# Performance work log

Hardware: AMD Instinct MI355X
Metric: run time of the kernel (lower is better)

The kernel has to match this reference:

```python
import jax, jax.numpy as jnp
import numpy as np

L, H, D, FF = 6, 12, 768, 3072  # num_layers, nhead, d_model, dim_feedforward
B, N = 4, 1024                  # batch, tokens
EPS = 1e-5                      # LayerNorm eps (torch default)


def setup_inputs() -> dict:
    key = jax.random.key(0)
    ks = jax.random.split(key, 6)
    s = 0.02
    return {
        "x": jax.random.normal(ks[0], (B, N, D), jnp.float32),
        "Wqkv": jax.random.normal(ks[1], (L, 3 * D, D), jnp.float32) * s,
        "bqkv": jnp.zeros((L, 3 * D), jnp.float32),
        "Wo": jax.random.normal(ks[2], (L, D, D), jnp.float32) * s,
        "bo": jnp.zeros((L, D), jnp.float32),
        "ln1_g": jnp.ones((L, D), jnp.float32),
        "ln1_b": jnp.zeros((L, D), jnp.float32),
        "ln2_g": jnp.ones((L, D), jnp.float32),
        "ln2_b": jnp.zeros((L, D), jnp.float32),
        "W1": jax.random.normal(ks[3], (L, FF, D), jnp.float32) * s,
        "b1": jnp.zeros((L, FF), jnp.float32),
        "W2": jax.random.normal(ks[4], (L, D, FF), jnp.float32) * s,
        "b2": jnp.zeros((L, D), jnp.float32),
    }


def _ln(x, g, b):
    m = jnp.mean(x, axis=-1, keepdims=True)
    v = jnp.var(x, axis=-1, keepdims=True)
    return (x - m) * jax.lax.rsqrt(v + EPS) * g + b


def _mha(x, Wqkv, bqkv, Wo, bo):
    # nn.MultiheadAttention with need_weights=True: explicit QK^T-softmax-AV path
    b_, n_, d_ = x.shape
    dh = d_ // H
    qkv = x @ Wqkv.T + bqkv                       # [B, N, 3D]
    q, k, v = jnp.split(qkv, 3, axis=-1)
    heads = lambda t: t.reshape(b_, n_, H, dh).transpose(0, 2, 1, 3)  # [B, H, N, dh]
    q, k, v = heads(q), heads(k), heads(v)
    scores = jnp.einsum('bhnd,bhmd->bhnm', q, k) / jnp.sqrt(jnp.float32(dh))
    attn = jax.nn.softmax(scores, axis=-1)        # [B, H, N, N] (the captured weights)
    out = jnp.einsum('bhnm,bhmd->bhnd', attn, v)
    out = out.transpose(0, 2, 1, 3).reshape(b_, n_, d_)
    return out @ Wo.T + bo


def reference(x, Wqkv, bqkv, Wo, bo, ln1_g, ln1_b, ln2_g, ln2_b, W1, b1, W2, b2):
    # Faithful to the custom forward: norm1 -> MHA -> residual -> norm1 again -> FFN -> residual -> norm2
    # dropout=0.0 (eval), so dropout layers are identity.
    for l in range(L):
        src = _ln(x, ln1_g[l], ln1_b[l])
        a = _mha(src, Wqkv[l], bqkv[l], Wo[l], bo[l])
        x = _ln(x + a, ln1_g[l], ln1_b[l])
        h = jax.nn.gelu(x @ W1[l].T + b1[l], approximate=False)  # torch 'gelu' = exact erf gelu
        x = _ln(x + h @ W2[l].T + b2[l], ln2_g[l], ln2_b[l])
    return x
```

## Files before the change

### kernel.cpp

```cpp
#include <hip/hip_runtime.h>
#include <math.h>

#define DEV __device__ __forceinline__

typedef __attribute__((ext_vector_type(4))) float f32x4;
typedef __attribute__((ext_vector_type(8))) __bf16 bf16x8;
typedef __attribute__((ext_vector_type(4))) unsigned short u16x4;
typedef __attribute__((ext_vector_type(8))) unsigned short u16x8;

enum {
  LAYERS = 6, NH = 12, DM = 768, FFD = 3072, BB = 4, NT = 1024,
  MM = BB * NT,
  TD = 3 * DM
};

DEV unsigned short f2bf(float f) {
  union { float f; unsigned u; } c; c.f = f;
  unsigned u = c.u;
  return (unsigned short)((u + 0x7fffu + ((u >> 16) & 1u)) >> 16);
}

DEV void gll16(const void* gsrc, void* ldst) {
  __builtin_amdgcn_global_load_lds(
      (const __attribute__((address_space(1))) unsigned int*)gsrc,
      (__attribute__((address_space(3))) unsigned int*)ldst, 16, 0, 0);
}

DEV f32x4 mfma16(bf16x8 a, bf16x8 b, f32x4 c) {
  return __builtin_amdgcn_mfma_f32_16x16x32_bf16(a, b, c, 0, 0, 0);
}

__global__ __launch_bounds__(256) void cvt_kernel(const f32x4* __restrict__ in,
                                                  u16x4* __restrict__ out, int n4) {
  int i = blockIdx.x * blockDim.x + threadIdx.x;
  int stride = gridDim.x * blockDim.x;
  for (; i < n4; i += stride) {
    f32x4 v = in[i];
    u16x4 o;
    o[0] = f2bf(v[0]); o[1] = f2bf(v[1]); o[2] = f2bf(v[2]); o[3] = f2bf(v[3]);
    out[i] = o;
  }
}

__global__ __launch_bounds__(256) void ln_kernel(const float* __restrict__ xin,
                                                 const float* __restrict__ ain,
                                                 const float* __restrict__ gam,
                                                 const float* __restrict__ bet,
                                                 float* __restrict__ xout,
                                                 unsigned short* __restrict__ bfout) {
  const int row  = blockIdx.x * 4 + (threadIdx.x >> 6);
  const int lane = threadIdx.x & 63;
  const f32x4* xr = (const f32x4*)(xin + (size_t)row * DM);
  f32x4 v[3];
#pragma unroll
  for (int p = 0; p < 3; p++) v[p] = xr[lane + 64 * p];
  if (ain) {
    const f32x4* ar = (const f32x4*)(ain + (size_t)row * DM);
#pragma unroll
    for (int p = 0; p < 3; p++) v[p] += ar[lane + 64 * p];
  }
  float s = 0.f, sq = 0.f;
#pragma unroll
  for (int p = 0; p < 3; p++)
#pragma unroll
    for (int j = 0; j < 4; j++) { float f = v[p][j]; s += f; sq += f * f; }
#pragma unroll
  for (int o = 1; o < 64; o <<= 1) {
    s  += __shfl_xor(s, o, 64);
    sq += __shfl_xor(sq, o, 64);
  }
  const float mean = s * (1.0f / DM);
  const float var  = sq * (1.0f / DM) - mean * mean;
  const float rstd = rsqrtf(var + 1e-5f);
  const f32x4* gr = (const f32x4*)gam;
  const f32x4* br = (const f32x4*)bet;
#pragma unroll
  for (int p = 0; p < 3; p++) {
    f32x4 gv = gr[lane + 64 * p];
    f32x4 bv = br[lane + 64 * p];
    f32x4 o = (v[p] - mean) * rstd * gv + bv;
    if (xout) ((f32x4*)(xout + (size_t)row * DM))[lane + 64 * p] = o;
    if (bfout) {
      u16x4 h;
      h[0] = f2bf(o[0]); h[1] = f2bf(o[1]); h[2] = f2bf(o[2]); h[3] = f2bf(o[3]);
      ((u16x4*)(bfout + (size_t)row * DM))[lane + 64 * p] = h;
    }
  }
}

template <int EPI, int TN>
__global__ __launch_bounds__(256) void gemm_bt(const unsigned short* __restrict__ A,
                                               const unsigned short* __restrict__ Wb,
                                               const float* __restrict__ bias,
                                               void* __restrict__ Cout,
                                               int Ksz, int Nsz) {
  constexpr int BN = TN / 32;
  __shared__ alignas(16) unsigned short As[128 * 32];
  __shared__ alignas(16) unsigned short Bs[TN * 32];

  const int t = threadIdx.x;
  const int lane = t & 63;
  const int w = t >> 6;
  const int g = lane >> 4;
  const int qi = lane & 15;
  const int wr = w >> 1;
  const int wc = w & 1;
  const int m0 = blockIdx.y * 128;
  const int n0 = blockIdx.x * TN;

  f32x4 acc[4][BN];
#pragma unroll
  for (int am = 0; am < 4; am++)
#pragma unroll
    for (int bn = 0; bn < BN; bn++) acc[am][bn] = (f32x4){0.f, 0.f, 0.f, 0.f};

  const int srow = t >> 2;
  const int schk = t & 3;
  const unsigned short* Ag = A  + (size_t)(m0 + srow) * Ksz + schk * 8;
  const unsigned short* Bg = Wb + (size_t)(n0 + srow) * Ksz + schk * 8;

  for (int kt = 0; kt < Ksz; kt += 32) {
    __syncthreads();
    gll16(Ag + kt,                    As + srow * 32 + schk * 8);
    gll16(Ag + (size_t)64 * Ksz + kt, As + (srow + 64) * 32 + schk * 8);
    gll16(Bg + kt,                    Bs + srow * 32 + schk * 8);
    if constexpr (TN == 128)
      gll16(Bg + (size_t)64 * Ksz + kt, Bs + (srow + 64) * 32 + schk * 8);
    __syncthreads();

    bf16x8 af[4], bfr[BN];
#pragma unroll
    for (int am = 0; am < 4; am++)
      af[am] = *(const bf16x8*)(As + (wr * 64 + am * 16 + qi) * 32 + g * 8);
#pragma unroll
    for (int bn = 0; bn < BN; bn++)
      bfr[bn] = *(const bf16x8*)(Bs + (wc * (TN / 2) + bn * 16 + qi) * 32 + g * 8);
#pragma unroll
    for (int am = 0; am < 4; am++)
#pragma unroll
      for (int bn = 0; bn < BN; bn++)
        acc[am][bn] = mfma16(af[am], bfr[bn], acc[am][bn]);
  }

  float bv[BN];
#pragma unroll
  for (int bn = 0; bn < BN; bn++)
    bv[bn] = bias[n0 + wc * (TN / 2) + bn * 16 + qi];

#pragma unroll
  for (int am = 0; am < 4; am++)
#pragma unroll
    for (int bn = 0; bn < BN; bn++)
#pragma unroll
      for (int r = 0; r < 4; r++) {
        const int mrow = m0 + wr * 64 + am * 16 + g * 4 + r;
        const int ncol = n0 + wc * (TN / 2) + bn * 16 + qi;
        float v = acc[am][bn][r] + bv[bn];
        if constexpr (EPI == 0) {
          ((float*)Cout)[(size_t)mrow * Nsz + ncol] = v;
        } else if constexpr (EPI == 1) {
          if (ncol < DM) v *= 0.125f;
          ((unsigned short*)Cout)[(size_t)mrow * Nsz + ncol] = f2bf(v);
        } else {
          v = 0.5f * v * (1.f + erff(v * 0.70710678118654752f));
          ((unsigned short*)Cout)[(size_t)mrow * Nsz + ncol] = f2bf(v);
        }
      }
}

__global__ __launch_bounds__(128) void attn_kernel(const unsigned short* __restrict__ qkv,
                                                   unsigned short* __restrict__ outp) {
  __shared__ alignas(16) unsigned short Ks[128 * 64];
  __shared__ alignas(16) unsigned short Vt[64 * 128];
  __shared__ alignas(16) unsigned short Ps[2][32 * 128];

  const int t = threadIdx.x;
  const int w = t >> 6;
  const int lane = t & 63;
  const int g = lane >> 4;
  const int qi = lane & 15;
  const int bidx = blockIdx.x;
  const int qtile = bidx & 15;
  const int bh = bidx >> 4;
  const int h = bh % NH;
  const int b = bh / NH;
  const int q0 = qtile * 64 + w * 32;
  const size_t base_bn = (size_t)b * NT;

  bf16x8 qf[2][2];
#pragma unroll
  for (int qt = 0; qt < 2; qt++)
#pragma unroll
    for (int kk = 0; kk < 2; kk++) {
      const int qrow = q0 + qt * 16 + qi;
      qf[qt][kk] = *(const bf16x8*)(qkv + (base_bn + qrow) * TD + h * 64 + kk * 32 + g * 8);
    }

  f32x4 oacc[2][4];
#pragma unroll
  for (int qt = 0; qt < 2; qt++)
#pragma unroll
    for (int dt = 0; dt < 4; dt++) oacc[qt][dt] = (f32x4){0.f, 0.f, 0.f, 0.f};
  float mval[2] = {-__builtin_inff(), -__builtin_inff()};
  float lval[2] = {0.f, 0.f};
  unsigned short* Pw = &Ps[w][0];

  for (int kv0 = 0; kv0 < NT; kv0 += 128) {
    __syncthreads();
#pragma unroll
    for (int rr = 0; rr < 8; rr++) {
      const int n = rr * 16 + (t >> 3);
      const int cd = t & 7;
      const int cg = cd ^ (n & 7);
      const unsigned short* src = qkv + (base_bn + kv0 + n) * TD + DM + h * 64 + cg * 8;
      gll16(src, Ks + n * 64 + cd * 8);
    }
#pragma unroll
    for (int r2 = 0; r2 < 2; r2++) {
      const int kb = t >> 3;
      const int d0 = r2 * 32 + (t & 7) * 4;
      u16x4 vv[8];
#pragma unroll
      for (int i = 0; i < 8; i++)
        vv[i] = *(const u16x4*)(qkv + (base_bn + kv0 + kb * 8 + i) * TD + 2 * DM + h * 64 + d0);
#pragma unroll
      for (int j = 0; j < 4; j++) {
        const int d = d0 + j;
        u16x8 w8;
#pragma unroll
        for (int i = 0; i < 8; i++) w8[i] = vv[i][j];
        *(u16x8*)((char*)Vt + d * 256 + ((kb ^ (d & 7)) * 16)) = w8;
      }
    }
    __syncthreads();

    f32x4 sacc[8][2];
#pragma unroll
    for (int nt = 0; nt < 8; nt++)
#pragma unroll
      for (int qt = 0; qt < 2; qt++) sacc[nt][qt] = (f32x4){0.f, 0.f, 0.f, 0.f};
#pragma unroll
    for (int nt = 0; nt < 8; nt++) {
      const int n = nt * 16 + qi;
      bf16x8 kf0 = *(const bf16x8*)((const char*)Ks + n * 128 + (((0 + g) ^ (n & 7)) * 16));
      bf16x8 kf1 = *(const bf16x8*)((const char*)Ks + n * 128 + (((4 + g) ^ (n & 7)) * 16));
#pragma unroll
      for (int qt = 0; qt < 2; qt++) {
        sacc[nt][qt] = mfma16(kf0, qf[qt][0], sacc[nt][qt]);
        sacc[nt][qt] = mfma16(kf1, qf[qt][1], sacc[nt][qt]);
      }
    }

#pragma unroll
    for (int qt = 0; qt < 2; qt++) {
      float mx = -__builtin_inff();
#pragma unroll
      for (int nt = 0; nt < 8; nt++)
#pragma unroll
        for (int r = 0; r < 4; r++) mx = fmaxf(mx, sacc[nt][qt][r]);
      mx = fmaxf(mx, __shfl_xor(mx, 16, 64));
      mx = fmaxf(mx, __shfl_xor(mx, 32, 64));
      const float mnew = fmaxf(mval[qt], mx);
      const float scl = __expf(mval[qt] - mnew);
      mval[qt] = mnew;
      float rsum = 0.f;
#pragma unroll
      for (int nt = 0; nt < 8; nt++)
#pragma unroll
        for (int r = 0; r < 4; r++) {
          const float p = __expf(sacc[nt][qt][r] - mnew);
          sacc[nt][qt][r] = p;
          rsum += p;
        }
      rsum += __shfl_xor(rsum, 16, 64);
      rsum += __shfl_xor(rsum, 32, 64);
      lval[qt] = lval[qt] * scl + rsum;
#pragma unroll
      for (int r = 0; r < 4; r++) {
        const float sr = __shfl(scl, g * 4 + r, 64);
#pragma unroll
        for (int dt = 0; dt < 4; dt++) oacc[qt][dt][r] *= sr;
      }
      const int qrow = qt * 16 + qi;
#pragma unroll
      for (int nt = 0; nt < 8; nt++) {
        u16x4 pk;
#pragma unroll
        for (int r = 0; r < 4; r++) pk[r] = f2bf(sacc[nt][qt][r]);
        const int byteoff = qrow * 256 + (((2 * nt + (g >> 1)) ^ (qrow & 7)) * 16) + (g & 1) * 8;
        *(u16x4*)((char*)Pw + byteoff) = pk;
      }
    }

#pragma unroll
    for (int kk2 = 0; kk2 < 4; kk2++) {
      bf16x8 pf[2], vf[4];
#pragma unroll
      for (int qt = 0; qt < 2; qt++) {
        const int qrow = qt * 16 + qi;
        pf[qt] = *(const bf16x8*)((const char*)Pw + qrow * 256 + (((kk2 * 4 + g) ^ (qrow & 7)) * 16));
      }
#pragma unroll
      for (int dt = 0; dt < 4; dt++) {
        const int d = dt * 16 + qi;
        vf[dt] = *(const bf16x8*)((const char*)Vt + d * 256 + (((kk2 * 4 + g) ^ (d & 7)) * 16));
      }
#pragma unroll
      for (int qt = 0; qt < 2; qt++)
#pragma unroll
        for (int dt = 0; dt < 4; dt++)
          oacc[qt][dt] = mfma16(pf[qt], vf[dt], oacc[qt][dt]);
    }
  }

#pragma unroll
  for (int qt = 0; qt < 2; qt++) {
    const float linv = 1.f / lval[qt];
#pragma unroll
    for (int r = 0; r < 4; r++) {
      const float lr = __shfl(linv, g * 4 + r, 64);
      const int qrow = q0 + qt * 16 + g * 4 + r;
#pragma unroll
      for (int dt = 0; dt < 4; dt++) {
        const float v = oacc[qt][dt][r] * lr;
        outp[(base_bn + qrow) * DM + h * 64 + dt * 16 + qi] = f2bf(v);
      }
    }
  }
}

extern "C" void kernel_launch(void* const* d_in, const int* in_sizes, int n_in,
                              void* d_out, int out_size, void* d_ws, size_t ws_size,
                              hipStream_t stream) {
  const float* x_in = (const float*)d_in[0];
  const float* Wqkv = (const float*)d_in[1];
  const float* bqkv = (const float*)d_in[2];
  const float* Wo   = (const float*)d_in[3];
  const float* bo   = (const float*)d_in[4];
  const float* ln1g = (const float*)d_in[5];
  const float* ln1b = (const float*)d_in[6];
  const float* ln2g = (const float*)d_in[7];
  const float* ln2b = (const float*)d_in[8];
  const float* W1   = (const float*)d_in[9];
  const float* b1   = (const float*)d_in[10];
  const float* W2   = (const float*)d_in[11];
  const float* b2   = (const float*)d_in[12];
  float* outp = (float*)d_out;

  char* ws = (char*)d_ws;
  size_t off = 0;
  auto alloc = [&](size_t bytes) {
    void* p = ws + off;
    off += (bytes + 255) & ~(size_t)255;
    return p;
  };
  unsigned short* wq_l = (unsigned short*)alloc((size_t)TD * DM * 2);
  unsigned short* wo_l = (unsigned short*)alloc((size_t)DM * DM * 2);
  unsigned short* w1_l = (unsigned short*)alloc((size_t)FFD * DM * 2);
  unsigned short* w2_l = (unsigned short*)alloc((size_t)DM * FFD * 2);
  unsigned short* src_bf  = (unsigned short*)alloc((size_t)MM * DM * 2);
  unsigned short* qkv_bf  = (unsigned short*)alloc((size_t)MM * TD * 2);
  unsigned short* attn_bf = (unsigned short*)alloc((size_t)MM * DM * 2);
  unsigned short* h_bf    = (unsigned short*)alloc((size_t)MM * FFD * 2);
  float* abuf             = (float*)alloc((size_t)MM * DM * 4);
  float* x_f32            = (float*)alloc((size_t)MM * DM * 4);

  for (int l = 0; l < LAYERS; l++) {
    const float* xcur = (l == 0) ? x_in : x_f32;
    cvt_kernel<<<512, 256, 0, stream>>>((const f32x4*)(Wqkv + (size_t)l * TD * DM),
                                        (u16x4*)wq_l, TD * DM / 4);
    cvt_kernel<<<512, 256, 0, stream>>>((const f32x4*)(Wo + (size_t)l * DM * DM),
                                        (u16x4*)wo_l, DM * DM / 4);
    cvt_kernel<<<512, 256, 0, stream>>>((const f32x4*)(W1 + (size_t)l * FFD * DM),
                                        (u16x4*)w1_l, FFD * DM / 4);
    cvt_kernel<<<512, 256, 0, stream>>>((const f32x4*)(W2 + (size_t)l * DM * FFD),
                                        (u16x4*)w2_l, DM * FFD / 4);

    ln_kernel<<<1024, 256, 0, stream>>>(xcur, nullptr, ln1g + l * DM, ln1b + l * DM,
                                        nullptr, src_bf);
    gemm_bt<1, 128><<<dim3(TD / 128, MM / 128), 256, 0, stream>>>(
        src_bf, wq_l, bqkv + l * TD, qkv_bf, DM, TD);
    attn_kernel<<<BB * NH * (NT / 64), 128, 0, stream>>>(qkv_bf, attn_bf);
    gemm_bt<0, 64><<<dim3(DM / 64, MM / 128), 256, 0, stream>>>(
        attn_bf, wo_l, bo + l * DM, abuf, DM, DM);
    ln_kernel<<<1024, 256, 0, stream>>>(xcur, abuf, ln1g + l * DM, ln1b + l * DM,
                                        x_f32, src_bf);
    gemm_bt<2, 128><<<dim3(FFD / 128, MM / 128), 256, 0, stream>>>(
        src_bf, w1_l, b1 + l * FFD, h_bf, DM, FFD);
    gemm_bt<0, 64><<<dim3(DM / 64, MM / 128), 256, 0, stream>>>(
        h_bf, w2_l, b2 + l * DM, abuf, FFD, DM);
    ln_kernel<<<1024, 256, 0, stream>>>(x_f32, abuf, ln2g + l * DM, ln2b + l * DM,
                                        (l == LAYERS - 1) ? outp : x_f32, nullptr);
  }
  (void)in_sizes; (void)n_in; (void)out_size; (void)ws_size;
}
```

Baseline: 1.626 ms.

## Split-K the D-output GEMMs, remap blocks across XCDs, batch weight conversions

The two GEMMs that produce D-wide outputs (Wo and W2) now split K in two along grid z. Each half writes its own fp32 partial buffer, and the following LayerNorm sums both partials with the residual. This doubles the block count for those underfilled 384-block grids. GEMM and attention block IDs are remapped so consecutive tiles land on the same XCD for L2 reuse. The four per-layer weight-conversion launches are merged into one kernel. The cost is twice the fp32 partial-output traffic plus one extra read in LayerNorm.

```diff
diff --git a/kernel.cpp b/kernel.cpp
--- a/kernel.cpp
+++ b/kernel.cpp
@@ -30,20 +30,42 @@
   return __builtin_amdgcn_mfma_f32_16x16x32_bf16(a, b, c, 0, 0, 0);
 }
 
-__global__ __launch_bounds__(256) void cvt_kernel(const f32x4* __restrict__ in,
-                                                  u16x4* __restrict__ out, int n4) {
-  int i = blockIdx.x * blockDim.x + threadIdx.x;
-  int stride = gridDim.x * blockDim.x;
-  for (; i < n4; i += stride) {
-    f32x4 v = in[i];
+DEV int xcd_remap(int id, int nwg) {
+  const int q = nwg >> 3, r = nwg & 7;
+  const int xcd = id & 7, j = id >> 3;
+  return (xcd < r ? xcd * (q + 1) : r * (q + 1) + (xcd - r) * q) + j;
+}
+
+__global__ __launch_bounds__(256) void cvt4_kernel(
+    const f32x4* __restrict__ i0, u16x4* __restrict__ o0, int c0,
+    const f32x4* __restrict__ i1, u16x4* __restrict__ o1, int c1,
+    const f32x4* __restrict__ i2, u16x4* __restrict__ o2, int c2,
+    const f32x4* __restrict__ i3, u16x4* __restrict__ o3, int c3) {
+  int i = blockIdx.x * 256 + threadIdx.x;
+  const int stride = gridDim.x * 256;
+  const int total = c0 + c1 + c2 + c3;
+  for (; i < total; i += stride) {
+    const f32x4* src; u16x4* dst; int k = i;
+    if (k < c0) { src = i0; dst = o0; }
+    else {
+      k -= c0;
+      if (k < c1) { src = i1; dst = o1; }
+      else {
+        k -= c1;
+        if (k < c2) { src = i2; dst = o2; }
+        else { k -= c2; src = i3; dst = o3; }
+      }
+    }
+    f32x4 v = src[k];
     u16x4 o;
     o[0] = f2bf(v[0]); o[1] = f2bf(v[1]); o[2] = f2bf(v[2]); o[3] = f2bf(v[3]);
-    out[i] = o;
+    dst[k] = o;
   }
 }
 
 __global__ __launch_bounds__(256) void ln_kernel(const float* __restrict__ xin,
                                                  const float* __restrict__ ain,
+                                                 const float* __restrict__ ain2,
                                                  const float* __restrict__ gam,
                                                  const float* __restrict__ bet,
                                                  float* __restrict__ xout,
@@ -56,6 +78,11 @@
   for (int p = 0; p < 3; p++) v[p] = xr[lane + 64 * p];
   if (ain) {
     const f32x4* ar = (const f32x4*)(ain + (size_t)row * DM);
+#pragma unroll
+    for (int p = 0; p < 3; p++) v[p] += ar[lane + 64 * p];
+  }
+  if (ain2) {
+    const f32x4* ar = (const f32x4*)(ain2 + (size_t)row * DM);
 #pragma unroll
     for (int p = 0; p < 3; p++) v[p] += ar[lane + 64 * p];
   }
@@ -98,6 +125,14 @@
   __shared__ alignas(16) unsigned short As[128 * 32];
   __shared__ alignas(16) unsigned short Bs[TN * 32];
 
+  const int gx = gridDim.x, gy = gridDim.y, gz = gridDim.z;
+  int id = blockIdx.x + gx * (blockIdx.y + gy * blockIdx.z);
+  id = xcd_remap(id, gx * gy * gz);
+  const int tz = id / (gx * gy);
+  const int rem = id - tz * (gx * gy);
+  const int ty = rem / gx;
+  const int tx = rem - ty * gx;
+
   const int t = threadIdx.x;
   const int lane = t & 63;
   const int w = t >> 6;
@@ -105,8 +140,11 @@
   const int qi = lane & 15;
   const int wr = w >> 1;
   const int wc = w & 1;
-  const int m0 = blockIdx.y * 128;
-  const int n0 = blockIdx.x * TN;
+  const int m0 = ty * 128;
+  const int n0 = tx * TN;
+  const int ksz_per = Ksz / gz;
+  const int k_begin = tz * ksz_per;
+  const int k_end = k_begin + ksz_per;
 
   f32x4 acc[4][BN];
 #pragma unroll
@@ -119,7 +157,7 @@
   const unsigned short* Ag = A  + (size_t)(m0 + srow) * Ksz + schk * 8;
   const unsigned short* Bg = Wb + (size_t)(n0 + srow) * Ksz + schk * 8;
 
-  for (int kt = 0; kt < Ksz; kt += 32) {
+  for (int kt = k_begin; kt < k_end; kt += 32) {
     __syncthreads();
     gll16(Ag + kt,                    As + srow * 32 + schk * 8);
     gll16(Ag + (size_t)64 * Ksz + kt, As + (srow + 64) * 32 + schk * 8);
@@ -145,7 +183,9 @@
   float bv[BN];
 #pragma unroll
   for (int bn = 0; bn < BN; bn++)
-    bv[bn] = bias[n0 + wc * (TN / 2) + bn * 16 + qi];
+    bv[bn] = (tz == 0) ? bias[n0 + wc * (TN / 2) + bn * 16 + qi] : 0.f;
+
+  float* Cf = (float*)Cout + (size_t)tz * ((size_t)gy * 128) * Nsz;
 
 #pragma unroll
   for (int am = 0; am < 4; am++)
@@ -157,7 +197,7 @@
         const int ncol = n0 + wc * (TN / 2) + bn * 16 + qi;
         float v = acc[am][bn][r] + bv[bn];
         if constexpr (EPI == 0) {
-          ((float*)Cout)[(size_t)mrow * Nsz + ncol] = v;
+          Cf[(size_t)mrow * Nsz + ncol] = v;
         } else if constexpr (EPI == 1) {
           if (ncol < DM) v *= 0.125f;
           ((unsigned short*)Cout)[(size_t)mrow * Nsz + ncol] = f2bf(v);
@@ -179,7 +219,7 @@
   const int lane = t & 63;
   const int g = lane >> 4;
   const int qi = lane & 15;
-  const int bidx = blockIdx.x;
+  const int bidx = xcd_remap(blockIdx.x, gridDim.x);
   const int qtile = bidx & 15;
   const int bh = bidx >> 4;
   const int h = bh % NH;
@@ -362,34 +402,35 @@
   unsigned short* qkv_bf  = (unsigned short*)alloc((size_t)MM * TD * 2);
   unsigned short* attn_bf = (unsigned short*)alloc((size_t)MM * DM * 2);
   unsigned short* h_bf    = (unsigned short*)alloc((size_t)MM * FFD * 2);
-  float* abuf             = (float*)alloc((size_t)MM * DM * 4);
+  float* abuf             = (float*)alloc((size_t)2 * MM * DM * 4);
   float* x_f32            = (float*)alloc((size_t)MM * DM * 4);
+  float* abuf1 = abuf + (size_t)MM * DM;
 
   for (int l = 0; l < LAYERS; l++) {
     const float* xcur = (l == 0) ? x_in : x_f32;
-    cvt_kernel<<<512, 256, 0, stream>>>((const f32x4*)(Wqkv + (size_t)l * TD * DM),
-                                        (u16x4*)wq_l, TD * DM / 4);
-    cvt_kernel<<<512, 256, 0, stream>>>((const f32x4*)(Wo + (size_t)l * DM * DM),
-                                        (u16x4*)wo_l, DM * DM / 4);
-    cvt_kernel<<<512, 256, 0, stream>>>((const f32x4*)(W1 + (size_t)l * FFD * DM),
-                                        (u16x4*)w1_l, FFD * DM / 4);
-    cvt_kernel<<<512, 256, 0, stream>>>((const f32x4*)(W2 + (size_t)l * DM * FFD),
-                                        (u16x4*)w2_l, DM * FFD / 4);
-
-    ln_kernel<<<1024, 256, 0, stream>>>(xcur, nullptr, ln1g + l * DM, ln1b + l * DM,
+    cvt4_kernel<<<1024, 256, 0, stream>>>(
+        (const f32x4*)(Wqkv + (size_t)l * TD * DM), (u16x4*)wq_l, TD * DM / 4,
+        (const f32x4*)(Wo   + (size_t)l * DM * DM), (u16x4*)wo_l, DM * DM / 4,
+        (const f32x4*)(W1   + (size_t)l * FFD * DM), (u16x4*)w1_l, FFD * DM / 4,
+        (const f32x4*)(W2   + (size_t)l * DM * FFD), (u16x4*)w2_l, DM * FFD / 4);
+
+    ln_kernel<<<1024, 256, 0, stream>>>(xcur, nullptr, nullptr,
+                                        ln1g + l * DM, ln1b + l * DM,
                                         nullptr, src_bf);
     gemm_bt<1, 128><<<dim3(TD / 128, MM / 128), 256, 0, stream>>>(
         src_bf, wq_l, bqkv + l * TD, qkv_bf, DM, TD);
     attn_kernel<<<BB * NH * (NT / 64), 128, 0, stream>>>(qkv_bf, attn_bf);
-    gemm_bt<0, 64><<<dim3(DM / 64, MM / 128), 256, 0, stream>>>(
+    gemm_bt<0, 64><<<dim3(DM / 64, MM / 128, 2), 256, 0, stream>>>(
         attn_bf, wo_l, bo + l * DM, abuf, DM, DM);
-    ln_kernel<<<1024, 256, 0, stream>>>(xcur, abuf, ln1g + l * DM, ln1b + l * DM,
+    ln_kernel<<<1024, 256, 0, stream>>>(xcur, abuf, abuf1,
+                                        ln1g + l * DM, ln1b + l * DM,
                                         x_f32, src_bf);
     gemm_bt<2, 128><<<dim3(FFD / 128, MM / 128), 256, 0, stream>>>(
         src_bf, w1_l, b1 + l * FFD, h_bf, DM, FFD);
-    gemm_bt<0, 64><<<dim3(DM / 64, MM / 128), 256, 0, stream>>>(
+    gemm_bt<0, 64><<<dim3(DM / 64, MM / 128, 2), 256, 0, stream>>>(
         h_bf, w2_l, b2 + l * DM, abuf, FFD, DM);
-    ln_kernel<<<1024, 256, 0, stream>>>(x_f32, abuf, ln2g + l * DM, ln2b + l * DM,
+    ln_kernel<<<1024, 256, 0, stream>>>(x_f32, abuf, abuf1,
+                                        ln2g + l * DM, ln2b + l * DM,
                                         (l == LAYERS - 1) ? outp : x_f32, nullptr);
   }
   (void)in_sizes; (void)n_in; (void)out_size; (void)ws_size;
```

New measurement: 1.395 ms. -14.3%, faster.
